# Kernel optimization log

Measured on AMD Instinct MI355X. Metric: run time of the kernel, lower is better.

Reference implementation:

```python
import jax, jax.numpy as jnp
import numpy as np

B, T, HID = 16, 512, 1024
NH, NKV, D = 8, 4, 128
THETA = 10000.0


def setup_inputs() -> dict:
    key = jax.random.key(0)
    k0, k1, k2, k3, k4 = jax.random.split(key, 5)
    s = 0.02
    return {
        "hidden_states": jax.random.normal(k0, (B, T, HID), dtype=jnp.float32),
        "Wq": s * jax.random.normal(k1, (HID, NH * D), dtype=jnp.float32),
        "Wk": s * jax.random.normal(k2, (HID, NKV * D), dtype=jnp.float32),
        "Wv": s * jax.random.normal(k3, (HID, NKV * D), dtype=jnp.float32),
        "Wo": s * jax.random.normal(k4, (NH * D, HID), dtype=jnp.float32),
    }


def _rotate_half(x):
    x1, x2 = x[..., : x.shape[-1] // 2], x[..., x.shape[-1] // 2:]
    return jnp.concatenate((-x2, x1), axis=-1)


def reference(hidden_states, Wq, Wk, Wv, Wo):
    b, t, _ = hidden_states.shape
    # projections -> [B, H, T, D]
    q = (hidden_states @ Wq).reshape(b, t, NH, D).transpose(0, 2, 1, 3)
    k = (hidden_states @ Wk).reshape(b, t, NKV, D).transpose(0, 2, 1, 3)
    v = (hidden_states @ Wv).reshape(b, t, NKV, D).transpose(0, 2, 1, 3)

    # RoPE: cos/sin [T, D]
    inv_freq = 1.0 / (THETA ** (jnp.arange(0, D, 2, dtype=jnp.float32) / D))
    freqs = jnp.outer(jnp.arange(t, dtype=jnp.float32), inv_freq)
    emb = jnp.concatenate((freqs, freqs), axis=-1)
    cos, sin = jnp.cos(emb), jnp.sin(emb)
    q = q * cos + _rotate_half(q) * sin
    k = k * cos + _rotate_half(k) * sin

    # repeat_interleave KV heads to match query heads (GQA)
    groups = NH // NKV
    k = jnp.repeat(k, groups, axis=1)  # [B, NH, T, D]
    v = jnp.repeat(v, groups, axis=1)

    scale = 1.0 / jnp.sqrt(jnp.float32(D))
    attn = jnp.einsum("bhtd,bhsd->bhts", q, k) * scale  # [B, NH, T, T]
    causal = jnp.triu(jnp.ones((t, t), dtype=bool), k=1)
    attn = jnp.where(causal, -jnp.inf, attn)
    attn = jax.nn.softmax(attn, axis=-1)  # dropout p=0 (eval)

    out = jnp.einsum("bhts,bhsd->bhtd", attn, v)
    out = out.transpose(0, 2, 1, 3).reshape(b, t, NH * D)
    return out @ Wo  # [B, T, HID]
```

## Files before the change

### kernel.cpp

```cpp
#include <hip/hip_runtime.h>
#include <hip/hip_bf16.h>
#include <math.h>

#define Bn 16
#define Tn 512
#define HIDn 1024
#define NHn 8
#define NKVn 4
#define Dn 128

typedef __attribute__((ext_vector_type(8))) short short8;
typedef __attribute__((ext_vector_type(4))) float floatx4;

__device__ __forceinline__ short bf16r(float f) {
  __hip_bfloat16 h = __float2bfloat16(f);
  return *(short*)&h;
}
__device__ __forceinline__ float bf16f(short s) {
  __hip_bfloat16 h = *(__hip_bfloat16*)&s;
  return __bfloat162float(h);
}

__device__ __forceinline__ void g2l16(const short* g, short* l) {
  __builtin_amdgcn_global_load_lds(
      (const __attribute__((address_space(1))) void*)g,
      (__attribute__((address_space(3))) void*)l, 16, 0, 0);
}

__global__ __launch_bounds__(256) void prep_kernel(const float* __restrict__ X,
                                                   const float* __restrict__ Wq,
                                                   const float* __restrict__ Wk,
                                                   const float* __restrict__ Wv,
                                                   const float* __restrict__ Wo,
                                                   short* __restrict__ Xb,
                                                   short* __restrict__ BtQKV,
                                                   short* __restrict__ Wot) {
  __shared__ float tile[32][33];
  int bid = blockIdx.x;
  if (bid < 4096) {
    int i = bid * 256 + threadIdx.x;
    const float4* p = reinterpret_cast<const float4*>(X) + (size_t)i * 2;
    float4 a = p[0], b = p[1];
    short8 o;
    o[0] = bf16r(a.x); o[1] = bf16r(a.y); o[2] = bf16r(a.z); o[3] = bf16r(a.w);
    o[4] = bf16r(b.x); o[5] = bf16r(b.y); o[6] = bf16r(b.z); o[7] = bf16r(b.w);
    reinterpret_cast<short8*>(Xb)[i] = o;
    return;
  }
  int t = bid - 4096;
  const float* in;
  short* out;
  int N;
  if (t < 1024)      { in = Wq; out = BtQKV;               N = 1024; }
  else if (t < 1536) { t -= 1024; in = Wk; out = BtQKV + 1024 * 1024; N = 512; }
  else if (t < 2048) { t -= 1536; in = Wv; out = BtQKV + 1536 * 1024; N = 512; }
  else               { t -= 2048; in = Wo; out = Wot;                N = 1024; }
  int ntx = N >> 5;
  int n0 = (t % ntx) * 32, k0 = (t / ntx) * 32;
  int tx = threadIdx.x & 31, ty = threadIdx.x >> 5;
  for (int i = 0; i < 32; i += 8)
    tile[ty + i][tx] = in[(size_t)(k0 + ty + i) * N + n0 + tx];
  __syncthreads();
  for (int i = 0; i < 32; i += 8)
    out[(size_t)(n0 + ty + i) * 1024 + k0 + tx] = bf16r(tile[tx][ty + i]);
}

__global__ __launch_bounds__(512, 2) void gemm_qkv(const short* __restrict__ A,
                                                   const short* __restrict__ Bt,
                                                   short* __restrict__ Cqkv,
                                                   short* __restrict__ Vt) {
  __shared__ __align__(16) short SH[65536];
  const int tid = threadIdx.x;
  const int wave = tid >> 6, lane = tid & 63;
  const int quad = lane >> 4, l16 = lane & 15;
  const int wr = wave >> 2, wc = wave & 3;
  int fid = blockIdx.y * 8 + blockIdx.x;
  int swz = (fid & 7) * 32 + (fid >> 3);
  const int bx = swz & 7;
  const int m0 = (swz >> 3) << 8, n0 = bx << 8;
  const int nt = 16;

  floatx4 acc[2][2][4][2];
#pragma unroll
  for (int r = 0; r < 2; ++r)
#pragma unroll
    for (int c = 0; c < 2; ++c)
#pragma unroll
      for (int mi = 0; mi < 4; ++mi)
#pragma unroll
        for (int ni = 0; ni < 2; ++ni)
          acc[r][c][mi][ni] = (floatx4){0.f, 0.f, 0.f, 0.f};

  const int srow = tid >> 3;
  const int schunk = (tid & 7) ^ (srow & 7);

#define STAGE(tile_, src_, row0_, ldso_)                                             \
  do {                                                                               \
    int t_ = (tile_);                                                                \
    if (t_ < nt) {                                                                   \
      short* bb_ = SH + ((t_ & 1) << 15) + (ldso_);                                  \
      const short* sp_ =                                                             \
          (src_) + ((size_t)((row0_) + srow) << 10) + (t_ << 6) + (schunk << 3);     \
      g2l16(sp_, bb_ + (wave << 9));                                                 \
      g2l16(sp_ + (64 << 10), bb_ + 4096 + (wave << 9));                             \
    }                                                                                \
  } while (0)

#define LDA(rhalf_)                                                                  \
  do {                                                                               \
    _Pragma("unroll") for (int mi = 0; mi < 4; ++mi) {                               \
      int R = (rhalf_) * 128 + wr * 64 + mi * 16 + l16;                              \
      _Pragma("unroll") for (int k = 0; k < 2; ++k) {                                \
        int pos = (k * 4 + quad) ^ (R & 7);                                          \
        af[mi][k] = *(const short8*)&Ab[R * 64 + pos * 8];                           \
      }                                                                              \
    }                                                                                \
  } while (0)

#define LDB(dst_, chalf_)                                                            \
  do {                                                                               \
    _Pragma("unroll") for (int ni = 0; ni < 2; ++ni) {                               \
      int R = (chalf_) * 128 + wc * 32 + ni * 16 + l16;                              \
      _Pragma("unroll") for (int k = 0; k < 2; ++k) {                                \
        int pos = (k * 4 + quad) ^ (R & 7);                                          \
        dst_[ni][k] = *(const short8*)&Bb[R * 64 + pos * 8];                         \
      }                                                                              \
    }                                                                                \
  } while (0)

#define MFMA_Q(r_, c_, bf_)                                                          \
  do {                                                                               \
    _Pragma("unroll") for (int mi = 0; mi < 4; ++mi)                                 \
        _Pragma("unroll") for (int ni = 0; ni < 2; ++ni) {                           \
      acc[r_][c_][mi][ni] = __builtin_amdgcn_mfma_f32_16x16x32_bf16(                 \
          af[mi][0], bf_[ni][0], acc[r_][c_][mi][ni], 0, 0, 0);                      \
      acc[r_][c_][mi][ni] = __builtin_amdgcn_mfma_f32_16x16x32_bf16(                 \
          af[mi][1], bf_[ni][1], acc[r_][c_][mi][ni], 0, 0, 0);                      \
    }                                                                                \
  } while (0)

#define PH_OPEN()                                                                    \
  do {                                                                               \
    __builtin_amdgcn_s_barrier();                                                    \
    asm volatile("s_waitcnt lgkmcnt(0)");                                            \
    __builtin_amdgcn_s_setprio(1);                                                   \
  } while (0)
#define PH_CLOSE()                                                                   \
  do {                                                                               \
    __builtin_amdgcn_s_setprio(0);                                                   \
    __builtin_amdgcn_s_barrier();                                                    \
  } while (0)

  STAGE(0, A, m0, 0);
  STAGE(0, Bt, n0 + 128, 24576);
  STAGE(0, Bt, n0, 16384);
  STAGE(0, A, m0 + 128, 8192);
  STAGE(1, A, m0, 0);
  STAGE(1, Bt, n0 + 128, 24576);
  STAGE(1, Bt, n0, 16384);
  asm volatile("s_waitcnt vmcnt(6)" ::: "memory");
  __builtin_amdgcn_s_barrier();

  short8 af[4][2], bf0[2][2], bf1[2][2];
  for (int g = 0; g < nt; ++g) {
    const short* Ab = SH + ((g & 1) << 15);
    const short* Bb = Ab + 16384;
    LDA(0);
    LDB(bf0, 0);
    STAGE(g + 1, A, m0 + 128, 8192);
    PH_OPEN();
    MFMA_Q(0, 0, bf0);
    PH_CLOSE();
    LDB(bf1, 1);
    STAGE(g + 2, A, m0, 0);
    PH_OPEN();
    MFMA_Q(0, 1, bf1);
    PH_CLOSE();
    LDA(1);
    STAGE(g + 2, Bt, n0 + 128, 24576);
    PH_OPEN();
    MFMA_Q(1, 1, bf1);
    PH_CLOSE();
    STAGE(g + 2, Bt, n0, 16384);
    PH_OPEN();
    MFMA_Q(1, 0, bf0);
    __builtin_amdgcn_s_setprio(0);
    if (g + 2 < nt)
      asm volatile("s_waitcnt vmcnt(6)" ::: "memory");
    else
      asm volatile("s_waitcnt vmcnt(0)" ::: "memory");
    __builtin_amdgcn_s_barrier();
  }

  if (bx < 6) {
#pragma unroll
    for (int r = 0; r < 2; ++r)
#pragma unroll
      for (int c = 0; c < 2; ++c)
#pragma unroll
        for (int mi = 0; mi < 4; ++mi)
#pragma unroll
          for (int ni = 0; ni < 2; ++ni)
#pragma unroll
            for (int rr = 0; rr < 4; ++rr) {
              int row = m0 + r * 128 + wr * 64 + mi * 16 + quad * 4 + rr;
              int col = n0 + c * 128 + wc * 32 + ni * 16 + l16;
              Cqkv[(size_t)row * 2048 + col] = bf16r(acc[r][c][mi][ni][rr]);
            }
  } else {
    const int b = m0 >> 9, t0 = m0 & (Tn - 1);
#pragma unroll
    for (int ch = 0; ch < 2; ++ch) {
      __syncthreads();
#pragma unroll
      for (int r = 0; r < 2; ++r)
#pragma unroll
        for (int mi = 0; mi < 4; ++mi)
#pragma unroll
          for (int ni = 0; ni < 2; ++ni)
#pragma unroll
            for (int rr = 0; rr < 4; ++rr) {
              int t = r * 128 + wr * 64 + mi * 16 + quad * 4 + rr;
              int d = wc * 32 + ni * 16 + l16;
              SH[d * 264 + t] = bf16r(acc[r][ch][mi][ni][rr]);
            }
      __syncthreads();
      int kv = (bx - 6) * 2 + ch;
#pragma unroll
      for (int u = 0; u < 8; ++u) {
        int idx = tid + u * 512;
        int d = idx >> 5, tb = (idx & 31) << 3;
        short8 vv = *(short8*)&SH[d * 264 + tb];
        *(short8*)&Vt[((size_t)(b * NKVn + kv) * 128 + d) * Tn + t0 + tb] = vv;
      }
    }
  }
#undef STAGE
#undef LDA
#undef LDB
#undef MFMA_Q
#undef PH_OPEN
#undef PH_CLOSE
}

__global__ void rope_k_kernel(short* __restrict__ C) {
  int idx = blockIdx.x * blockDim.x + threadIdx.x;
  int vec = idx & 7;
  int head = (idx >> 3) & 3;
  int bt = idx >> 5;
  int t = bt & (Tn - 1);
  int i0 = vec * 8;
  size_t base = (size_t)bt * 2048 + 1024 + head * 128 + i0;
  short8 x1 = *(short8*)&C[base];
  short8 x2 = *(short8*)&C[base + 64];
  short8 o1, o2;
  float tf = (float)t;
#pragma unroll
  for (int j = 0; j < 8; ++j) {
    float a = tf * exp2f(-0.2076205059f * (float)(i0 + j));
    float s, c;
    sincosf(a, &s, &c);
    float v1 = bf16f(x1[j]), v2 = bf16f(x2[j]);
    o1[j] = bf16r(v1 * c - v2 * s);
    o2[j] = bf16r(v2 * c + v1 * s);
  }
  *(short8*)&C[base] = o1;
  *(short8*)&C[base + 64] = o2;
}

template <bool OUTF32>
__global__ __launch_bounds__(256) void gemm_bt(const short* __restrict__ A,
                                               const short* __restrict__ Bt,
                                               void* __restrict__ Cout,
                                               int M, int N, int K) {
  __shared__ __align__(16) short As[128 * 64];
  __shared__ __align__(16) short Bs[128 * 64];
  const int tid = threadIdx.x;
  const int wave = tid >> 6, lane = tid & 63;
  const int quad = lane >> 4, l16 = lane & 15;
  const int wrow = wave >> 1, wcol = wave & 1;
  const int m0 = blockIdx.y * 128, n0 = blockIdx.x * 128;
  floatx4 acc[4][4];
  for (int mi = 0; mi < 4; ++mi)
    for (int ni = 0; ni < 4; ++ni)
      acc[mi][ni] = (floatx4){0.f, 0.f, 0.f, 0.f};

  for (int kt = 0; kt < K; kt += 64) {
#pragma unroll
    for (int v = 0; v < 4; ++v) {
      int s = tid + v * 256;
      int r = s >> 3;
      int c = (s & 7) ^ (r & 7);
      short* dstA = (short*)As + (size_t)(v * 256 + wave * 64) * 8;
      g2l16(&A[(size_t)(m0 + r) * K + kt + c * 8], dstA);
      short* dstB = (short*)Bs + (size_t)(v * 256 + wave * 64) * 8;
      g2l16(&Bt[(size_t)(n0 + r) * K + kt + c * 8], dstB);
    }
    __syncthreads();
#pragma unroll
    for (int kc = 0; kc < 2; ++kc) {
      short8 af[4], bfr[4];
#pragma unroll
      for (int mi = 0; mi < 4; ++mi) {
        int R = wrow * 64 + mi * 16 + l16;
        int pos = (kc * 4 + quad) ^ (R & 7);
        af[mi] = *(short8*)&As[R * 64 + pos * 8];
      }
#pragma unroll
      for (int ni = 0; ni < 4; ++ni) {
        int R = wcol * 64 + ni * 16 + l16;
        int pos = (kc * 4 + quad) ^ (R & 7);
        bfr[ni] = *(short8*)&Bs[R * 64 + pos * 8];
      }
#pragma unroll
      for (int mi = 0; mi < 4; ++mi)
#pragma unroll
        for (int ni = 0; ni < 4; ++ni)
          acc[mi][ni] = __builtin_amdgcn_mfma_f32_16x16x32_bf16(af[mi], bfr[ni], acc[mi][ni], 0, 0, 0);
    }
    __syncthreads();
  }
#pragma unroll
  for (int mi = 0; mi < 4; ++mi)
#pragma unroll
    for (int ni = 0; ni < 4; ++ni)
#pragma unroll
      for (int r = 0; r < 4; ++r) {
        int row = m0 + wrow * 64 + mi * 16 + quad * 4 + r;
        int col = n0 + wcol * 64 + ni * 16 + l16;
        if (OUTF32)
          ((float*)Cout)[(size_t)row * N + col] = acc[mi][ni][r];
        else
          ((short*)Cout)[(size_t)row * N + col] = bf16r(acc[mi][ni][r]);
      }
}

__global__ __launch_bounds__(256) void attn_kernel(const short* __restrict__ Cqkv,
                                                   const short* __restrict__ Vt,
                                                   short* __restrict__ Aout) {
  __shared__ __align__(16) short SH[37376];
  short* Ks = SH;
  short* Vs = SH + 16384;
  short (*Ps)[16][72] = reinterpret_cast<short(*)[16][72]>(SH + 32768);
  const int tid = threadIdx.x;
  const int wave = tid >> 6, lane = tid & 63;
  const int quad = lane >> 4, l16 = lane & 15;
  const int blk = blockIdx.x;
  const int qt = 7 - (blk >> 7);
  const int h = blk & 7, b = (blk >> 3) & 15;
  const int kvh = h >> 1;
  const short* Qp = Cqkv + (size_t)b * Tn * 2048 + h * 128;
  const short* Kp = Cqkv + (size_t)b * Tn * 2048 + 1024 + kvh * 128;
  const short* Vtp = Vt + (size_t)(b * NKVn + kvh) * 128 * Tn;

  const int qrow0 = qt * 64 + wave * 16;
  const float scale = 0.12753378904f;

#define STAGEKV(k0_, b_)                                                      \
  do {                                                                        \
    _Pragma("unroll") for (int v = 0; v < 4; ++v) {                           \
      int s_ = tid + v * 256;                                                 \
      int r_ = s_ >> 4, c_ = (s_ & 15) ^ (r_ & 15);                           \
      g2l16(&Kp[(size_t)((k0_) + r_) * 2048 + c_ * 8],                        \
            Ks + ((b_) << 13) + (v * 256 + wave * 64) * 8);                   \
    }                                                                         \
    _Pragma("unroll") for (int v = 0; v < 4; ++v) {                           \
      int s_ = tid + v * 256;                                                 \
      int r_ = s_ >> 3, c_ = (s_ & 7) ^ (r_ & 7);                             \
      g2l16(&Vtp[(size_t)r_ * Tn + (k0_) + c_ * 8],                           \
            Vs + ((b_) << 13) + (v * 256 + wave * 64) * 8);                   \
    }                                                                         \
  } while (0)

  short8 qf[4];
#pragma unroll
  for (int kc = 0; kc < 4; ++kc)
    qf[kc] = *(const short8*)&Qp[(size_t)(qrow0 + l16) * 2048 + kc * 32 + quad * 8];

  STAGEKV(0, 0);

  {
    float tf = (float)(qrow0 + l16);
#pragma unroll
    for (int kc = 0; kc < 2; ++kc)
#pragma unroll
      for (int j = 0; j < 8; ++j) {
        int d = kc * 32 + quad * 8 + j;
        float a = tf * exp2f(-0.2076205059f * (float)d);
        float s, c;
        sincosf(a, &s, &c);
        float x1 = bf16f(qf[kc][j]), x2 = bf16f(qf[kc + 2][j]);
        qf[kc][j] = bf16r((x1 * c - x2 * s) * scale);
        qf[kc + 2][j] = bf16r((x2 * c + x1 * s) * scale);
      }
  }

  floatx4 o[8];
  float l_part[4];
#pragma unroll
  for (int ni = 0; ni < 8; ++ni) o[ni] = (floatx4){0.f, 0.f, 0.f, 0.f};
#pragma unroll
  for (int r = 0; r < 4; ++r) l_part[r] = 0.f;

  const int ntiles = qt + 1;
  __syncthreads();

  for (int it = 0; it < ntiles; ++it) {
    const int k0 = it << 6;
    const int cb = (it & 1) << 13;
    const short* Kb = Ks + cb;
    const short* Vb = Vs + cb;

    if (it + 1 < ntiles) STAGEKV(k0 + 64, (it + 1) & 1);

    floatx4 s[4];
    __builtin_amdgcn_s_setprio(1);
#pragma unroll
    for (int ni = 0; ni < 4; ++ni) {
      s[ni] = (floatx4){0.f, 0.f, 0.f, 0.f};
      short8 kf[4];
#pragma unroll
      for (int kc = 0; kc < 4; ++kc) {
        int R = ni * 16 + l16;
        int pos = (kc * 4 + quad) ^ (R & 15);
        kf[kc] = *(short8*)&Kb[R * 128 + pos * 8];
      }
#pragma unroll
      for (int kc = 0; kc < 4; ++kc)
        s[ni] = __builtin_amdgcn_mfma_f32_16x16x32_bf16(qf[kc], kf[kc], s[ni], 0, 0, 0);
    }
    __builtin_amdgcn_s_setprio(0);

    const bool diag = (k0 + 63 > qrow0);
#pragma unroll
    for (int ni = 0; ni < 4; ++ni)
#pragma unroll
      for (int r = 0; r < 4; ++r) {
        float p = exp2f(s[ni][r]);
        if (diag) {
          int key = k0 + ni * 16 + l16;
          int qr = qrow0 + quad * 4 + r;
          if (key > qr) p = 0.f;
        }
        s[ni][r] = p;
        l_part[r] += p;
      }

#pragma unroll
    for (int ni = 0; ni < 4; ++ni)
#pragma unroll
      for (int r = 0; r < 4; ++r)
        Ps[wave][quad * 4 + r][ni * 16 + l16] = bf16r(s[ni][r]);

    short8 pf[2];
#pragma unroll
    for (int kc = 0; kc < 2; ++kc)
      pf[kc] = *(short8*)&Ps[wave][l16][kc * 32 + quad * 8];
    __builtin_amdgcn_s_setprio(1);
#pragma unroll
    for (int ni = 0; ni < 8; ++ni) {
      int R = ni * 16 + l16;
      int pos0 = quad ^ (R & 7);
      int pos1 = (4 + quad) ^ (R & 7);
      short8 vf0 = *(short8*)&Vb[R * 64 + pos0 * 8];
      short8 vf1 = *(short8*)&Vb[R * 64 + pos1 * 8];
      o[ni] = __builtin_amdgcn_mfma_f32_16x16x32_bf16(pf[0], vf0, o[ni], 0, 0, 0);
      o[ni] = __builtin_amdgcn_mfma_f32_16x16x32_bf16(pf[1], vf1, o[ni], 0, 0, 0);
    }
    __builtin_amdgcn_s_setprio(0);

    if (it + 1 < ntiles) __syncthreads();
  }
#undef STAGEKV

  float inv[4];
#pragma unroll
  for (int r = 0; r < 4; ++r) {
    float rs = l_part[r];
#pragma unroll
    for (int off = 8; off >= 1; off >>= 1) rs += __shfl_xor(rs, off, 16);
    inv[r] = 1.0f / rs;
  }
#pragma unroll
  for (int ni = 0; ni < 8; ++ni)
#pragma unroll
    for (int r = 0; r < 4; ++r) {
      int t = qrow0 + quad * 4 + r;
      int d = ni * 16 + l16;
      Aout[((size_t)b * Tn + t) * 1024 + h * 128 + d] = bf16r(o[ni][r] * inv[r]);
    }
}

extern "C" void kernel_launch(void* const* d_in, const int* in_sizes, int n_in,
                              void* d_out, int out_size, void* d_ws, size_t ws_size,
                              hipStream_t stream) {
  const float* X  = (const float*)d_in[0];
  const float* Wq = (const float*)d_in[1];
  const float* Wk = (const float*)d_in[2];
  const float* Wv = (const float*)d_in[3];
  const float* Wo = (const float*)d_in[4];

  char* ws = (char*)d_ws;
  short* Xb    = (short*)(ws);
  short* BtQKV = (short*)(ws + (16ull << 20));
  short* Wot   = (short*)(ws + (20ull << 20));
  short* Cqkv  = (short*)(ws + (22ull << 20));
  short* Vt    = (short*)(ws + (54ull << 20));
  short* Aout  = (short*)(ws + (62ull << 20));

  prep_kernel<<<7168, 256, 0, stream>>>(X, Wq, Wk, Wv, Wo, Xb, BtQKV, Wot);
  gemm_qkv<<<dim3(8, 32), 512, 0, stream>>>(Xb, BtQKV, Cqkv, Vt);
  rope_k_kernel<<<1024, 256, 0, stream>>>(Cqkv);
  attn_kernel<<<1024, 256, 0, stream>>>(Cqkv, Vt, Aout);
  gemm_bt<true><<<dim3(8, 64), 256, 0, stream>>>(Aout, Wot, d_out, 8192, 1024, 1024);
}
```

Baseline: 187.7 us.

## Replace output GEMM with double-buffered 256x128 pipelined kernel

```diff
diff --git a/kernel.cpp b/kernel.cpp
--- a/kernel.cpp
+++ b/kernel.cpp
@@ -268,71 +268,138 @@
   *(short8*)&C[base + 64] = o2;
 }
 
-template <bool OUTF32>
-__global__ __launch_bounds__(256) void gemm_bt(const short* __restrict__ A,
-                                               const short* __restrict__ Bt,
-                                               void* __restrict__ Cout,
-                                               int M, int N, int K) {
-  __shared__ __align__(16) short As[128 * 64];
-  __shared__ __align__(16) short Bs[128 * 64];
+__global__ __launch_bounds__(512, 2) void gemm_out(const short* __restrict__ A,
+                                                   const short* __restrict__ Bt,
+                                                   float* __restrict__ Cout) {
+  __shared__ __align__(16) short SH[49152];
   const int tid = threadIdx.x;
   const int wave = tid >> 6, lane = tid & 63;
   const int quad = lane >> 4, l16 = lane & 15;
-  const int wrow = wave >> 1, wcol = wave & 1;
-  const int m0 = blockIdx.y * 128, n0 = blockIdx.x * 128;
-  floatx4 acc[4][4];
-  for (int mi = 0; mi < 4; ++mi)
-    for (int ni = 0; ni < 4; ++ni)
-      acc[mi][ni] = (floatx4){0.f, 0.f, 0.f, 0.f};
-
-  for (int kt = 0; kt < K; kt += 64) {
-#pragma unroll
-    for (int v = 0; v < 4; ++v) {
-      int s = tid + v * 256;
-      int r = s >> 3;
-      int c = (s & 7) ^ (r & 7);
-      short* dstA = (short*)As + (size_t)(v * 256 + wave * 64) * 8;
-      g2l16(&A[(size_t)(m0 + r) * K + kt + c * 8], dstA);
-      short* dstB = (short*)Bs + (size_t)(v * 256 + wave * 64) * 8;
-      g2l16(&Bt[(size_t)(n0 + r) * K + kt + c * 8], dstB);
-    }
-    __syncthreads();
-#pragma unroll
-    for (int kc = 0; kc < 2; ++kc) {
-      short8 af[4], bfr[4];
-#pragma unroll
-      for (int mi = 0; mi < 4; ++mi) {
-        int R = wrow * 64 + mi * 16 + l16;
-        int pos = (kc * 4 + quad) ^ (R & 7);
-        af[mi] = *(short8*)&As[R * 64 + pos * 8];
-      }
-#pragma unroll
-      for (int ni = 0; ni < 4; ++ni) {
-        int R = wcol * 64 + ni * 16 + l16;
-        int pos = (kc * 4 + quad) ^ (R & 7);
-        bfr[ni] = *(short8*)&Bs[R * 64 + pos * 8];
-      }
-#pragma unroll
-      for (int mi = 0; mi < 4; ++mi)
-#pragma unroll
-        for (int ni = 0; ni < 4; ++ni)
-          acc[mi][ni] = __builtin_amdgcn_mfma_f32_16x16x32_bf16(af[mi], bfr[ni], acc[mi][ni], 0, 0, 0);
-    }
-    __syncthreads();
-  }
-#pragma unroll
-  for (int mi = 0; mi < 4; ++mi)
-#pragma unroll
-    for (int ni = 0; ni < 4; ++ni)
-#pragma unroll
-      for (int r = 0; r < 4; ++r) {
-        int row = m0 + wrow * 64 + mi * 16 + quad * 4 + r;
-        int col = n0 + wcol * 64 + ni * 16 + l16;
-        if (OUTF32)
-          ((float*)Cout)[(size_t)row * N + col] = acc[mi][ni][r];
-        else
-          ((short*)Cout)[(size_t)row * N + col] = bf16r(acc[mi][ni][r]);
-      }
+  const int wr = wave >> 2, wc = wave & 3;
+  int fid = blockIdx.y * 8 + blockIdx.x;
+  int swz = (fid & 7) * 32 + (fid >> 3);
+  const int m0 = (swz >> 3) << 8;
+  const int n0 = (swz & 7) << 7;
+  const int nt = 16;
+
+  floatx4 acc[2][4][2];
+#pragma unroll
+  for (int r = 0; r < 2; ++r)
+#pragma unroll
+    for (int mi = 0; mi < 4; ++mi)
+#pragma unroll
+      for (int ni = 0; ni < 2; ++ni)
+        acc[r][mi][ni] = (floatx4){0.f, 0.f, 0.f, 0.f};
+
+  const int srow = tid >> 3;
+  const int schunk = (tid & 7) ^ (srow & 7);
+
+#define STAGE(tile_, src_, row0_, ldso_)                                             \
+  do {                                                                               \
+    int t_ = (tile_);                                                                \
+    if (t_ < nt) {                                                                   \
+      short* bb_ = SH + (t_ & 1) * 24576 + (ldso_);                                  \
+      const short* sp_ =                                                             \
+          (src_) + ((size_t)((row0_) + srow) << 10) + (t_ << 6) + (schunk << 3);     \
+      g2l16(sp_, bb_ + (wave << 9));                                                 \
+      g2l16(sp_ + (64 << 10), bb_ + 4096 + (wave << 9));                             \
+    }                                                                                \
+  } while (0)
+
+#define LDA(rhalf_)                                                                  \
+  do {                                                                               \
+    _Pragma("unroll") for (int mi = 0; mi < 4; ++mi) {                               \
+      int R = (rhalf_) * 128 + wr * 64 + mi * 16 + l16;                              \
+      _Pragma("unroll") for (int k = 0; k < 2; ++k) {                                \
+        int pos = (k * 4 + quad) ^ (R & 7);                                          \
+        af[mi][k] = *(const short8*)&Ab[R * 64 + pos * 8];                           \
+      }                                                                              \
+    }                                                                                \
+  } while (0)
+
+#define LDB()                                                                        \
+  do {                                                                               \
+    _Pragma("unroll") for (int ni = 0; ni < 2; ++ni) {                               \
+      int R = wc * 32 + ni * 16 + l16;                                               \
+      _Pragma("unroll") for (int k = 0; k < 2; ++k) {                                \
+        int pos = (k * 4 + quad) ^ (R & 7);                                          \
+        bf0[ni][k] = *(const short8*)&Bb[R * 64 + pos * 8];                          \
+      }                                                                              \
+    }                                                                                \
+  } while (0)
+
+#define MFMA_Q(r_)                                                                   \
+  do {                                                                               \
+    _Pragma("unroll") for (int mi = 0; mi < 4; ++mi)                                 \
+        _Pragma("unroll") for (int ni = 0; ni < 2; ++ni) {                           \
+      acc[r_][mi][ni] = __builtin_amdgcn_mfma_f32_16x16x32_bf16(                     \
+          af[mi][0], bf0[ni][0], acc[r_][mi][ni], 0, 0, 0);                          \
+      acc[r_][mi][ni] = __builtin_amdgcn_mfma_f32_16x16x32_bf16(                     \
+          af[mi][1], bf0[ni][1], acc[r_][mi][ni], 0, 0, 0);                          \
+    }                                                                                \
+  } while (0)
+
+#define PH_OPEN()                                                                    \
+  do {                                                                               \
+    __builtin_amdgcn_s_barrier();                                                    \
+    asm volatile("s_waitcnt lgkmcnt(0)");                                            \
+    __builtin_amdgcn_s_setprio(1);                                                   \
+  } while (0)
+#define PH_CLOSE()                                                                   \
+  do {                                                                               \
+    __builtin_amdgcn_s_setprio(0);                                                   \
+    __builtin_amdgcn_s_barrier();                                                    \
+  } while (0)
+
+  STAGE(0, A, m0, 0);
+  STAGE(0, Bt, n0, 16384);
+  STAGE(0, A, m0 + 128, 8192);
+  STAGE(1, A, m0, 0);
+  STAGE(1, Bt, n0, 16384);
+  asm volatile("s_waitcnt vmcnt(4)" ::: "memory");
+  __builtin_amdgcn_s_barrier();
+
+  short8 af[4][2], bf0[2][2];
+  for (int g = 0; g < nt; ++g) {
+    const short* Ab = SH + (g & 1) * 24576;
+    const short* Bb = Ab + 16384;
+    LDA(0);
+    LDB();
+    STAGE(g + 1, A, m0 + 128, 8192);
+    PH_OPEN();
+    MFMA_Q(0);
+    PH_CLOSE();
+    LDA(1);
+    STAGE(g + 2, A, m0, 0);
+    STAGE(g + 2, Bt, n0, 16384);
+    PH_OPEN();
+    MFMA_Q(1);
+    __builtin_amdgcn_s_setprio(0);
+    if (g + 2 < nt)
+      asm volatile("s_waitcnt vmcnt(4)" ::: "memory");
+    else
+      asm volatile("s_waitcnt vmcnt(0)" ::: "memory");
+    __builtin_amdgcn_s_barrier();
+  }
+
+#pragma unroll
+  for (int r = 0; r < 2; ++r)
+#pragma unroll
+    for (int mi = 0; mi < 4; ++mi)
+#pragma unroll
+      for (int ni = 0; ni < 2; ++ni)
+#pragma unroll
+        for (int rr = 0; rr < 4; ++rr) {
+          int row = m0 + r * 128 + wr * 64 + mi * 16 + quad * 4 + rr;
+          int col = n0 + wc * 32 + ni * 16 + l16;
+          Cout[(size_t)row * 1024 + col] = acc[r][mi][ni][rr];
+        }
+#undef STAGE
+#undef LDA
+#undef LDB
+#undef MFMA_Q
+#undef PH_OPEN
+#undef PH_CLOSE
 }
 
 __global__ __launch_bounds__(256) void attn_kernel(const short* __restrict__ Cqkv,
@@ -512,5 +579,5 @@
   gemm_qkv<<<dim3(8, 32), 512, 0, stream>>>(Xb, BtQKV, Cqkv, Vt);
   rope_k_kernel<<<1024, 256, 0, stream>>>(Cqkv);
   attn_kernel<<<1024, 256, 0, stream>>>(Cqkv, Vt, Aout);
-  gemm_bt<true><<<dim3(8, 64), 256, 0, stream>>>(Aout, Wot, d_out, 8192, 1024, 1024);
-}
+  gemm_out<<<dim3(8, 32), 512, 0, stream>>>(Aout, Wot, (float*)d_out);
+}
```

Measured after the change: 182.3 us. 2.9% less time.
